# Performance work log

Measured on AMD Instinct MI355X. Metric: run time of the kernel, lower is better.

The kernel has to match this reference:

```python
import jax, jax.numpy as jnp
import numpy as np

NEG_SLOPE = 0.2
LN_EPS = 1e-5


def _gat(x, src, dst, ea, Wl, Wr, We, att, b, heads, ch, concat):
    # GATv2 conv with edge features (eval mode: dropout = identity).
    N = x.shape[0]
    xl = (x @ Wl).reshape(N, heads, ch)          # source transform (also skip output)
    xr = (x @ Wr).reshape(N, heads, ch)          # target transform
    ee = (ea @ We).reshape(ea.shape[0], heads, ch)
    g = jax.nn.leaky_relu(xl[src] + xr[dst] + ee, NEG_SLOPE)   # [E,H,C]
    score = jnp.einsum('ehc,hc->eh', g, att)                    # [E,H]
    # segment softmax over destination nodes
    smax = jax.ops.segment_max(score, dst, num_segments=N)
    ex = jnp.exp(score - smax[dst])
    den = jax.ops.segment_sum(ex, dst, num_segments=N)
    alpha = ex / (den[dst] + 1e-16)
    out = jax.ops.segment_sum(xl[src] * alpha[..., None], dst, num_segments=N)  # [N,H,C]
    out = out.reshape(N, heads * ch) if concat else out.mean(axis=1)
    return out + b, xl.reshape(N, heads * ch)


def setup_inputs() -> dict:
    B, N, E, F, ED = 4, 20000, 640000, 64, 16
    HID, H1 = 16, 8
    key = jax.random.key(0)
    ks = jax.random.split(key, 32)

    def p(k, shape, fan):
        return (jax.random.normal(k, shape, jnp.float32) / np.float32(np.sqrt(fan)))

    inp = {
        'x': jax.random.normal(ks[0], (B, N, F), jnp.float32),
        'edge_attr': jax.random.normal(ks[1], (B, E, ED), jnp.float32),
        'edge_index': jax.random.randint(ks[2], (B, 2, E), 0, N, jnp.int32),
        # conv1: in=64, heads=8, out=16, concat
        'c1_Wl': p(ks[3], (F, H1 * HID), F),
        'c1_Wr': p(ks[4], (F, H1 * HID), F),
        'c1_We': p(ks[5], (ED, H1 * HID), ED),
        'c1_att': p(ks[6], (H1, HID), HID),
        'c1_b': jnp.zeros((H1 * HID,), jnp.float32),
        # conv2: in=128, heads=1, out=16, mean
        'c2_Wl': p(ks[7], (H1 * HID, HID), H1 * HID),
        'c2_Wr': p(ks[8], (H1 * HID, HID), H1 * HID),
        'c2_We': p(ks[9], (ED, HID), ED),
        'c2_att': p(ks[10], (1, HID), HID),
        'c2_b': jnp.zeros((HID,), jnp.float32),
        # skip_conv: in=128, heads=1, out=16, mean
        's_Wl': p(ks[11], (H1 * HID, HID), H1 * HID),
        's_Wr': p(ks[12], (H1 * HID, HID), H1 * HID),
        's_We': p(ks[13], (ED, HID), ED),
        's_att': p(ks[14], (1, HID), HID),
        's_b': jnp.zeros((HID,), jnp.float32),
        # lin_skip_conv + LayerNorm(16)
        'lin_W': p(ks[15], (HID, HID), HID),
        'lin_b': jnp.zeros((HID,), jnp.float32),
        'ln_g': jnp.ones((HID,), jnp.float32),
        'ln_b': jnp.zeros((HID,), jnp.float32),
    }
    return inp


def reference(x, edge_attr, edge_index,
              c1_Wl, c1_Wr, c1_We, c1_att, c1_b,
              c2_Wl, c2_Wr, c2_We, c2_att, c2_b,
              s_Wl, s_Wr, s_We, s_att, s_b,
              lin_W, lin_b, ln_g, ln_b):
    def single(xg, eig, eag):
        src, dst = eig[0], eig[1]
        h, skip = _gat(xg, src, dst, eag, c1_Wl, c1_Wr, c1_We, c1_att, c1_b, 8, 16, True)
        hx = jax.nn.elu(h)                                   # [N,128]
        x1, _ = _gat(hx, src, dst, eag, c2_Wl, c2_Wr, c2_We, c2_att, c2_b, 1, 16, False)
        # skip conv consumes hx with the residual skip features from conv1
        x2, _ = _gat(hx + skip, src, dst, eag, s_Wl, s_Wr, s_We, s_att, s_b, 1, 16, False)
        x2 = x2 @ lin_W.T + lin_b
        y = x1 + x2                                          # [N,16]
        mu = y.mean(-1, keepdims=True)
        var = ((y - mu) ** 2).mean(-1, keepdims=True)
        return (y - mu) / jnp.sqrt(var + LN_EPS) * ln_g + ln_b
    return jax.vmap(single)(x, edge_index, edge_attr)
```

## Files before the change

kernel.cpp:

```cpp
#include <hip/hip_runtime.h>
#include <hip/hip_bf16.h>

typedef __hip_bfloat16 bf16;
typedef float f32x2 __attribute__((ext_vector_type(2)));

#define NB_B 4
#define N 20000
#define E 640000
#define F 64
#define HC 128
#define ED 16
#define CH 16
#define NT 32
#define TB1 64
#define TB2 16

__device__ __forceinline__ float clampf(float v, float lo, float hi){ return fminf(fmaxf(v, lo), hi); }
__device__ __forceinline__ float ldv(const float* p, size_t i){ return p[i]; }
__device__ __forceinline__ float ldv(const bf16*  p, size_t i){ return __bfloat162float(p[i]); }
__device__ __forceinline__ void  stv(float* p, size_t i, float v){ p[i] = v; }
__device__ __forceinline__ void  stv(bf16*  p, size_t i, float v){ p[i] = __float2bfloat16(v); }
__device__ __forceinline__ unsigned short tobf(float v){ bf16 b = __float2bfloat16(v); return *(unsigned short*)&b; }
__device__ __forceinline__ float unpl(unsigned u){ return __uint_as_float(u << 16); }
__device__ __forceinline__ float unph(unsigned u){ return __uint_as_float(u & 0xffff0000u); }
__device__ __forceinline__ f32x2 mk2(float a, float b){ f32x2 r; r.x = a; r.y = b; return r; }

__device__ __forceinline__ float rsum16(float x){
  x += __int_as_float(__builtin_amdgcn_update_dpp(0, __float_as_int(x), 0x128, 0xf, 0xf, true));
  x += __int_as_float(__builtin_amdgcn_update_dpp(0, __float_as_int(x), 0x124, 0xf, 0xf, true));
  x += __int_as_float(__builtin_amdgcn_update_dpp(0, __float_as_int(x), 0x122, 0xf, 0xf, true));
  x += __int_as_float(__builtin_amdgcn_update_dpp(0, __float_as_int(x), 0x121, 0xf, 0xf, true));
  return x;
}

__global__ __launch_bounds__(256) void k_detect(const unsigned short* __restrict__ xu, int* __restrict__ flag){
  __shared__ int cnt[256];
  int tid = threadIdx.x;
  unsigned short lo = xu[2*tid];
  bf16 h = *(const bf16*)&lo;
  float v = fabsf(__bfloat162float(h));
  cnt[tid] = (v > 1e4f || (v != 0.f && v < 1e-4f)) ? 1 : 0;
  __syncthreads();
  for (int s=128; s>0; s>>=1){ if (tid<s) cnt[tid]+=cnt[tid+s]; __syncthreads(); }
  if (tid==0) *flag = (cnt[0] > 64) ? 1 : 0;
}

__global__ __launch_bounds__(256) void k_hist(const int* __restrict__ ei, int* __restrict__ cnt, int b0){
  int z = blockIdx.z, b = b0 + z;
  int e = blockIdx.x*256 + threadIdx.x;
  int d = ei[((size_t)b*2+1)*E + e];
  atomicAdd(&cnt[z*N + d], 1);
}

__global__ __launch_bounds__(256) void k_scan(const int* __restrict__ cnt, int* __restrict__ rowptr,
                                              int* __restrict__ cursor){
  int z = blockIdx.z, tid = threadIdx.x;
  const int* c = cnt + (size_t)z*N;
  int* rp = rowptr + (size_t)z*(N+1);
  int* cu = cursor + (size_t)z*N;
  const int CHK = (N + 255)/256;
  int lo = tid*CHK; int hi = lo + CHK; if (hi > N) hi = N; if (lo > N) lo = N;
  int s = 0;
  for (int i=lo;i<hi;i++) s += c[i];
  __shared__ int buf[256];
  buf[tid] = s; __syncthreads();
  for (int off=1; off<256; off<<=1){
    int t = (tid>=off) ? buf[tid-off] : 0;
    __syncthreads();
    buf[tid] += t;
    __syncthreads();
  }
  int run = buf[tid] - s;
  for (int i=lo;i<hi;i++){ int v=c[i]; rp[i]=run; cu[i]=run; run += v; }
  if (tid==255) rp[N] = run;
}

template<typename T>
__device__ __forceinline__ void scatter_body(const int* ei, int* cursor, int* csr,
                                             const T* ea, float* eacsr, int b0){
  int z = blockIdx.z, b = b0 + z;
  int e = blockIdx.x*256 + threadIdx.x;
  int s = ei[((size_t)b*2+0)*E + e];
  int d = ei[((size_t)b*2+1)*E + e];
  int pos = atomicAdd(&cursor[z*N + d], 1);
  csr[(size_t)z*E + pos] = s;
  float4* dst = (float4*)(eacsr + ((size_t)z*E + pos)*ED);
  const T* sp = ea + ((size_t)b*E + e)*ED;
  #pragma unroll
  for (int g=0; g<4; g++){
    float4 t;
    t.x = ldv(sp, g*4+0); t.y = ldv(sp, g*4+1); t.z = ldv(sp, g*4+2); t.w = ldv(sp, g*4+3);
    dst[g] = t;
  }
}
__global__ __launch_bounds__(256) void k_scatter(const int* ei, int* cursor, int* csr,
    const void* ea, float* eacsr, const int* flag, int b0){
  if (*flag) scatter_body(ei, cursor, csr, (const float*)ea, eacsr, b0);
  else       scatter_body(ei, cursor, csr, (const bf16*) ea, eacsr, b0);
}

template<typename T>
__device__ __forceinline__ void node1_body(const T* x, const T* Wl, const T* Wr,
                                           unsigned* xl1p, unsigned* xr1p, int b0,
                                           float (*xs)[F+4]){
  int z = blockIdx.z, b = b0 + z;
  int node0 = blockIdx.x*NT;
  for (int i=threadIdx.x; i<NT*F; i+=256){
    int n = i>>6, k = i&63;
    xs[n][k] = ldv(x, ((size_t)b*N + node0 + n)*F + k);
  }
  __syncthreads();
  int mat = threadIdx.x >> 7, c = threadIdx.x & 127;
  const T* W = mat ? Wr : Wl;
  float acc[NT];
  #pragma unroll
  for (int n=0;n<NT;n++) acc[n]=0.f;
  for (int k=0;k<F;k+=4){
    float w0 = ldv(W, (size_t)(k+0)*HC + c);
    float w1 = ldv(W, (size_t)(k+1)*HC + c);
    float w2 = ldv(W, (size_t)(k+2)*HC + c);
    float w3 = ldv(W, (size_t)(k+3)*HC + c);
    #pragma unroll
    for (int n=0;n<NT;n++){
      float4 xv = *(const float4*)&xs[n][k];
      acc[n] += xv.x*w0 + xv.y*w1 + xv.z*w2 + xv.w*w3;
    }
  }
  unsigned short* outp = (unsigned short*)(mat ? xr1p : xl1p);
  int half = c>>6, cc = c&63;
  #pragma unroll
  for (int n=0;n<NT;n++){
    float v = clampf(acc[n], -1e4f, 1e4f);
    outp[(((size_t)z*N + node0 + n)*64 + cc)*2 + half] = tobf(v);
  }
}
__global__ __launch_bounds__(256) void k_node1(const void* x, const void* Wl, const void* Wr,
    unsigned* xl1p, unsigned* xr1p, const int* flag, int b0){
  __shared__ float xs[NT][F+4];
  if (*flag) node1_body((const float*)x,(const float*)Wl,(const float*)Wr,xl1p,xr1p,b0,xs);
  else       node1_body((const bf16*) x,(const bf16*) Wl,(const bf16*) Wr,xl1p,xr1p,b0,xs);
}

template<typename T>
__device__ __forceinline__ void gather1_body(const int* rowptr, const int* csr, const float* eacsr,
    const T* We, const T* att, const T* b1,
    const unsigned* xl1p, const unsigned* xr1p, float* hx, int b0,
    int (*ssrc)[TB1], float (*eas)[TB1][16]){
  int z = blockIdx.z;
  int wid = threadIdx.x >> 6, lane = threadIdx.x & 63;
  int node = blockIdx.x*4 + wid;
  int rs = rowptr[(size_t)z*(N+1) + node];
  int re = rowptr[(size_t)z*(N+1) + node + 1];
  unsigned xru = xr1p[((size_t)z*N + node)*64 + lane];
  f32x2 xr2 = mk2(unpl(xru), unph(xru));
  f32x2 w[ED];
  #pragma unroll
  for (int j=0;j<ED;j++) w[j] = mk2(ldv(We, (size_t)j*HC + lane), ldv(We, (size_t)j*HC + lane + 64));
  f32x2 attv = mk2(ldv(att, (size_t)lane), ldv(att, (size_t)lane + 64));
  f32x2 acc = mk2(0.f,0.f), den = mk2(0.f,0.f);
  const unsigned* xlp = xl1p + (size_t)z*N*64;
  const int* csrz = csr + (size_t)z*E;

  auto edge = [&](int i, unsigned xw){
    f32x2 xl = mk2(unpl(xw), unph(xw));
    float ev[16];
    const float4* er = (const float4*)eas[wid][i];
    *(float4*)&ev[0]  = er[0];
    *(float4*)&ev[4]  = er[1];
    *(float4*)&ev[8]  = er[2];
    *(float4*)&ev[12] = er[3];
    f32x2 g = xl + xr2;
    #pragma unroll
    for (int j=0;j<ED;j++) g += w[j]*ev[j];
    f32x2 lr;
    lr.x = fmaxf(g.x,0.f) + 0.2f*fminf(g.x,0.f);
    lr.y = fmaxf(g.y,0.f) + 0.2f*fminf(g.y,0.f);
    f32x2 v = lr*attv;
    float vL = rsum16(v.x);
    float vH = rsum16(v.y);
    f32x2 ex = mk2(__expf(clampf(vL,-60.f,60.f)), __expf(clampf(vH,-60.f,60.f)));
    den += ex;
    acc += ex*xl;
  };

  for (int base = rs; base < re; base += TB1){
    int m = re - base; if (m > TB1) m = TB1;
    if (lane < m) ssrc[wid][lane] = csrz[base + lane];
    const float4* ep = (const float4*)(eacsr + ((size_t)z*E + base)*ED);
    for (int i4=lane; i4<m*4; i4+=64)
      *(float4*)&eas[wid][i4>>2][(i4&3)*4] = ep[i4];
    unsigned pa = xlp[(unsigned)(ssrc[wid][0]*64 + lane)];
    unsigned pb = (m>1) ? xlp[(unsigned)(ssrc[wid][1]*64 + lane)] : pa;
    int i = 0;
    for (; i+1 < m; i += 2){
      unsigned x0 = pa, x1 = pb;
      int i2 = (i+2 < m) ? i+2 : m-1;
      int i3 = (i+3 < m) ? i+3 : m-1;
      int s2 = ssrc[wid][i2], s3 = ssrc[wid][i3];
      pa = xlp[(unsigned)(s2*64 + lane)];
      pb = xlp[(unsigned)(s3*64 + lane)];
      edge(i, x0);
      edge(i+1, x1);
    }
    if (i < m) edge(i, pa);
  }
  float hL = acc.x/(den.x + 1e-16f) + ldv(b1, (size_t)lane);
  float hH = acc.y/(den.y + 1e-16f) + ldv(b1, (size_t)lane + 64);
  hL = hL>0.f ? hL : expm1f(hL);
  hH = hH>0.f ? hH : expm1f(hH);
  hx[((size_t)z*N + node)*HC + lane]      = hL;
  hx[((size_t)z*N + node)*HC + lane + 64] = hH;
}
__global__ __launch_bounds__(256) void k_gather1(const int* rowptr, const int* csr, const float* eacsr,
    const void* We, const void* att, const void* b1,
    const unsigned* xl1p, const unsigned* xr1p, float* hx, const int* flag, int b0){
  __shared__ int ssrc[4][TB1];
  __shared__ float eas[4][TB1][16];
  if (*flag) gather1_body(rowptr,csr,eacsr,(const float*)We,(const float*)att,(const float*)b1,xl1p,xr1p,hx,b0,ssrc,eas);
  else       gather1_body(rowptr,csr,eacsr,(const bf16*) We,(const bf16*) att,(const bf16*) b1,xl1p,xr1p,hx,b0,ssrc,eas);
}

template<typename T>
__device__ __forceinline__ void node2_body(const float* hx, const unsigned* xl1p,
    const T* W2l, const T* W2r, const T* W3l, const T* W3r,
    unsigned* xl23p, unsigned* xr23p, int b0,
    float (*hv)[HC+4], float (*sv)[HC+4]){
  int z = blockIdx.z;
  int node0 = blockIdx.x*NT;
  for (int i=threadIdx.x; i<NT*HC; i+=256){
    int n = i>>7, k = i&127;
    float h = hx[((size_t)z*N + node0 + n)*HC + k];
    unsigned wxl = xl1p[((size_t)z*N + node0 + n)*64 + (k&63)];
    float xv = (k<64) ? unpl(wxl) : unph(wxl);
    hv[n][k] = h;
    sv[n][k] = h + xv;
  }
  __syncthreads();
  int o = threadIdx.x & 63;
  int mat = o >> 4, c = o & 15;
  int g = threadIdx.x >> 6;
  const T* W = (mat==0)? W2l : (mat==1)? W2r : (mat==2)? W3l : W3r;
  float (*src)[HC+4] = (mat<2)? hv : sv;
  float acc[8];
  #pragma unroll
  for (int j=0;j<8;j++) acc[j]=0.f;
  for (int k=0;k<HC;k+=4){
    float w0 = ldv(W, (size_t)(k+0)*CH + c);
    float w1 = ldv(W, (size_t)(k+1)*CH + c);
    float w2 = ldv(W, (size_t)(k+2)*CH + c);
    float w3 = ldv(W, (size_t)(k+3)*CH + c);
    #pragma unroll
    for (int j=0;j<8;j++){
      float4 xv = *(const float4*)&src[g*8+j][k];
      acc[j] += xv.x*w0 + xv.y*w1 + xv.z*w2 + xv.w*w3;
    }
  }
  unsigned short* arr = (unsigned short*)((mat&1) ? xr23p : xl23p);
  int half = mat>>1;
  #pragma unroll
  for (int j=0;j<8;j++){
    float v = clampf(acc[j], -1e4f, 1e4f);
    arr[(((size_t)z*N + node0 + g*8 + j)*CH + c)*2 + half] = tobf(v);
  }
}
__global__ __launch_bounds__(256) void k_node2(const float* hx, const unsigned* xl1p,
    const void* W2l, const void* W2r, const void* W3l, const void* W3r,
    unsigned* xl23p, unsigned* xr23p, const int* flag, int b0){
  __shared__ float hv[NT][HC+4];
  __shared__ float sv[NT][HC+4];
  if (*flag) node2_body(hx,xl1p,(const float*)W2l,(const float*)W2r,(const float*)W3l,(const float*)W3r,xl23p,xr23p,b0,hv,sv);
  else       node2_body(hx,xl1p,(const bf16*) W2l,(const bf16*) W2r,(const bf16*) W3l,(const bf16*) W3r,xl23p,xr23p,b0,hv,sv);
}

template<typename T>
__device__ __forceinline__ void gather23_body(const int* rowptr, const int* csr, const float* eacsr,
    const T* We2, const T* We3, const T* att2, const T* att3,
    const T* b2, const T* b3, const T* linW, const T* linb, const T* lng, const T* lnb,
    const unsigned* xl23p, const unsigned* xr23p,
    T* out, int b0, int (*ssrc)[TB2], float (*eas)[TB2][16]){
  int z = blockIdx.z;
  int slot = threadIdx.x >> 4;
  int node = blockIdx.x*16 + slot;
  int c = threadIdx.x & 15;
  int rs = rowptr[(size_t)z*(N+1) + node];
  int re = rowptr[(size_t)z*(N+1) + node + 1];
  unsigned xru = xr23p[((size_t)z*N + node)*CH + c];
  f32x2 xr2 = mk2(unpl(xru), unph(xru));
  f32x2 w[ED];
  #pragma unroll
  for (int j=0;j<ED;j++) w[j] = mk2(ldv(We2,(size_t)j*CH+c), ldv(We3,(size_t)j*CH+c));
  f32x2 attv = mk2(ldv(att2,(size_t)c), ldv(att3,(size_t)c));
  f32x2 acc = mk2(0.f,0.f), den = mk2(0.f,0.f);
  const unsigned* xlp = xl23p + (size_t)z*N*CH;
  const int* csrz = csr + (size_t)z*E;

  auto edge = [&](int i, unsigned xw){
    f32x2 xl = mk2(unpl(xw), unph(xw));
    float ev[16];
    const float4* er = (const float4*)eas[slot][i];
    *(float4*)&ev[0]  = er[0];
    *(float4*)&ev[4]  = er[1];
    *(float4*)&ev[8]  = er[2];
    *(float4*)&ev[12] = er[3];
    f32x2 g = xl + xr2;
    #pragma unroll
    for (int j=0;j<ED;j++) g += w[j]*ev[j];
    f32x2 lr;
    lr.x = fmaxf(g.x,0.f) + 0.2f*fminf(g.x,0.f);
    lr.y = fmaxf(g.y,0.f) + 0.2f*fminf(g.y,0.f);
    f32x2 v = lr*attv;
    float v2 = rsum16(v.x);
    float v3 = rsum16(v.y);
    f32x2 ex = mk2(__expf(clampf(v2,-60.f,60.f)), __expf(clampf(v3,-60.f,60.f)));
    den += ex;
    acc += ex*xl;
  };

  for (int base = rs; base < re; base += TB2){
    int m = re - base; if (m > TB2) m = TB2;
    if (c < m) ssrc[slot][c] = csrz[base + c];
    const float4* ep = (const float4*)(eacsr + ((size_t)z*E + base)*ED);
    for (int i4=c; i4<m*4; i4+=16)
      *(float4*)&eas[slot][i4>>2][(i4&3)*4] = ep[i4];
    unsigned pa = xlp[(unsigned)(ssrc[slot][0]*CH + c)];
    unsigned pb = (m>1) ? xlp[(unsigned)(ssrc[slot][1]*CH + c)] : pa;
    int i = 0;
    for (; i+1 < m; i += 2){
      unsigned x0 = pa, x1 = pb;
      int i2 = (i+2 < m) ? i+2 : m-1;
      int i3 = (i+3 < m) ? i+3 : m-1;
      int s2 = ssrc[slot][i2], s3 = ssrc[slot][i3];
      pa = xlp[(unsigned)(s2*CH + c)];
      pb = xlp[(unsigned)(s3*CH + c)];
      edge(i, x0);
      edge(i+1, x1);
    }
    if (i < m) edge(i, pa);
  }
  float x1 = acc.x/(den.x + 1e-16f) + ldv(b2,(size_t)c);
  float x3 = acc.y/(den.y + 1e-16f) + ldv(b3,(size_t)c);
  float x2 = 0.f;
  #pragma unroll
  for (int j=0;j<16;j++) x2 += __shfl(x3, j, 16) * ldv(linW, (size_t)c*16 + j);
  x2 += ldv(linb,(size_t)c);
  float y = clampf(x1, -1e6f, 1e6f) + clampf(x2, -1e6f, 1e6f);
  float mu = rsum16(y)*(1.f/16.f);
  float dv = y - mu;
  float var = rsum16(dv*dv)*(1.f/16.f);
  float o = dv*rsqrtf(var + 1e-5f)*ldv(lng,(size_t)c) + ldv(lnb,(size_t)c);
  stv(out, ((size_t)(b0+z)*N + node)*16 + c, o);
}
__global__ __launch_bounds__(256) void k_gather23(const int* rowptr, const int* csr, const float* eacsr,
    const void* We2, const void* We3, const void* att2, const void* att3,
    const void* b2, const void* b3, const void* linW, const void* linb, const void* lng, const void* lnb,
    const unsigned* xl23p, const unsigned* xr23p,
    void* out, const int* flag, int b0){
  __shared__ int ssrc[16][TB2];
  __shared__ float eas[16][TB2][16];
  if (*flag) gather23_body(rowptr,csr,eacsr,(const float*)We2,(const float*)We3,(const float*)att2,(const float*)att3,
                           (const float*)b2,(const float*)b3,(const float*)linW,(const float*)linb,(const float*)lng,(const float*)lnb,
                           xl23p,xr23p,(float*)out,b0,ssrc,eas);
  else       gather23_body(rowptr,csr,eacsr,(const bf16*) We2,(const bf16*) We3,(const bf16*) att2,(const bf16*) att3,
                           (const bf16*) b2,(const bf16*) b3,(const bf16*) linW,(const bf16*) linb,(const bf16*) lng,(const bf16*) lnb,
                           xl23p,xr23p,(bf16*) out,b0,ssrc,eas);
}

struct WSP {
  int* flag;
  int *cnt, *cursor, *rowptr; int* csr;
  float *eacsr, *hx;
  unsigned *xl1p,*xr1p,*xl23p,*xr23p;
  size_t total;
};
static WSP mkws(char* base, int nb){
  WSP w; size_t off = 0;
  auto A = [&](size_t bytes)->char*{ char* p = base ? base + off : (char*)0; off = (off + bytes + 255) & ~(size_t)255; return p; };
  w.flag   = (int*)     A(256);
  w.cnt    = (int*)     A((size_t)nb*N*4);
  w.cursor = (int*)     A((size_t)nb*N*4);
  w.rowptr = (int*)     A((size_t)nb*(N+1)*4);
  w.csr    = (int*)     A((size_t)nb*E*4);
  w.eacsr  = (float*)   A((size_t)nb*E*ED*4);
  w.hx     = (float*)   A((size_t)nb*N*HC*4);
  w.xl1p   = (unsigned*)A((size_t)nb*N*64*4);
  w.xr1p   = (unsigned*)A((size_t)nb*N*64*4);
  w.xl23p  = (unsigned*)A((size_t)nb*N*CH*4);
  w.xr23p  = (unsigned*)A((size_t)nb*N*CH*4);
  w.total = off;
  return w;
}

extern "C" void kernel_launch(void* const* d_in, const int* in_sizes, int n_in,
                              void* d_out, int out_size, void* d_ws, size_t ws_size,
                              hipStream_t stream){
  const void* x    = d_in[0];
  const void* ea   = d_in[1];
  const int*  ei   = (const int*)d_in[2];
  const void* c1Wl = d_in[3], *c1Wr = d_in[4], *c1We = d_in[5];
  const void* c1att= d_in[6], *c1b  = d_in[7];
  const void* c2Wl = d_in[8], *c2Wr = d_in[9], *c2We = d_in[10];
  const void* c2att= d_in[11],*c2b  = d_in[12];
  const void* sWl  = d_in[13],*sWr  = d_in[14],*sWe  = d_in[15];
  const void* satt = d_in[16],*sb   = d_in[17];
  const void* linW = d_in[18],*linb = d_in[19];
  const void* lng  = d_in[20],*lnb  = d_in[21];

  auto run = [&](int b0, int nb){
    WSP w = mkws((char*)d_ws, nb);
    hipMemsetAsync(w.cnt, 0, (size_t)nb*N*4, stream);
    k_hist   <<<dim3(E/256,1,nb),   256,0,stream>>>(ei, w.cnt, b0);
    k_scan   <<<dim3(1,1,nb),       256,0,stream>>>(w.cnt, w.rowptr, w.cursor);
    k_scatter<<<dim3(E/256,1,nb),   256,0,stream>>>(ei, w.cursor, w.csr, ea, w.eacsr, w.flag, b0);
    k_node1  <<<dim3(N/NT,1,nb),    256,0,stream>>>(x, c1Wl, c1Wr, w.xl1p, w.xr1p, w.flag, b0);
    k_gather1<<<dim3(N/4,1,nb),     256,0,stream>>>(w.rowptr, w.csr, w.eacsr, c1We, c1att, c1b,
                                                    w.xl1p, w.xr1p, w.hx, w.flag, b0);
    k_node2  <<<dim3(N/NT,1,nb),    256,0,stream>>>(w.hx, w.xl1p, c2Wl, c2Wr, sWl, sWr,
                                                    w.xl23p, w.xr23p, w.flag, b0);
    k_gather23<<<dim3(N/16,1,nb),   256,0,stream>>>(w.rowptr, w.csr, w.eacsr, c2We, sWe, c2att, satt,
                                                    c2b, sb, linW, linb, lng, lnb,
                                                    w.xl23p, w.xr23p, d_out, w.flag, b0);
  };

  {
    WSP w0 = mkws((char*)d_ws, 1);
    k_detect<<<1,256,0,stream>>>((const unsigned short*)x, w0.flag);
  }

  WSP probe = mkws((char*)0, NB_B);
  if (ws_size >= probe.total){
    run(0, NB_B);
  } else {
    for (int g=0; g<NB_B; ++g) run(g, 1);
  }
}
```

Before: 1.130 ms.

## Drop LDS staging in gather kernels and split gather23 edges across wave sub-groups

Both gather kernels stop staging source indices and edge attributes in shared memory. They now read them directly from global memory with wave-uniform readfirstlane scalar loads and register prefetch of the next edge. gather23 now gives each node a full wave, with four 16-lane groups each taking every fourth edge, and combines their partial sums with shuffles. Exponentials switch to exp2 with log2(e) folded into the attention weights. This trades LDS traffic and barriers for more parallel memory requests per node, and it launches four times as many blocks for gather23, so lanes sit idle on low-degree nodes.

```diff
diff --git a/kernel.cpp b/kernel.cpp
--- a/kernel.cpp
+++ b/kernel.cpp
@@ -12,8 +12,6 @@
 #define ED 16
 #define CH 16
 #define NT 32
-#define TB1 64
-#define TB2 16
 
 __device__ __forceinline__ float clampf(float v, float lo, float hi){ return fminf(fmaxf(v, lo), hi); }
 __device__ __forceinline__ float ldv(const float* p, size_t i){ return p[i]; }
@@ -24,6 +22,9 @@
 __device__ __forceinline__ float unpl(unsigned u){ return __uint_as_float(u << 16); }
 __device__ __forceinline__ float unph(unsigned u){ return __uint_as_float(u & 0xffff0000u); }
 __device__ __forceinline__ f32x2 mk2(float a, float b){ f32x2 r; r.x = a; r.y = b; return r; }
+__device__ __forceinline__ int rfl(int v){ return __builtin_amdgcn_readfirstlane(v); }
+
+#define L2E 1.44269504f
 
 __device__ __forceinline__ float rsum16(float x){
   x += __int_as_float(__builtin_amdgcn_update_dpp(0, __float_as_int(x), 0x128, 0xf, 0xf, true));
@@ -142,82 +143,72 @@
 }
 
 template<typename T>
-__device__ __forceinline__ void gather1_body(const int* rowptr, const int* csr, const float* eacsr,
-    const T* We, const T* att, const T* b1,
-    const unsigned* xl1p, const unsigned* xr1p, float* hx, int b0,
-    int (*ssrc)[TB1], float (*eas)[TB1][16]){
+__device__ __forceinline__ void gather1_body(const int* __restrict__ rowptr, const int* __restrict__ csr,
+    const float* __restrict__ eacsr, const T* __restrict__ We, const T* __restrict__ att, const T* __restrict__ b1,
+    const unsigned* __restrict__ xl1p, const unsigned* __restrict__ xr1p, float* __restrict__ hx, int b0){
   int z = blockIdx.z;
-  int wid = threadIdx.x >> 6, lane = threadIdx.x & 63;
-  int node = blockIdx.x*4 + wid;
-  int rs = rowptr[(size_t)z*(N+1) + node];
-  int re = rowptr[(size_t)z*(N+1) + node + 1];
+  int lane = threadIdx.x & 63;
+  int node = rfl(blockIdx.x*4 + (threadIdx.x >> 6));
+  int rs = rfl(rowptr[(size_t)z*(N+1) + node]);
+  int re = rfl(rowptr[(size_t)z*(N+1) + node + 1]);
+  f32x2 w[ED];
+  #pragma unroll
+  for (int j=0;j<ED;j++) w[j] = mk2(ldv(We,(size_t)j*HC+lane), ldv(We,(size_t)j*HC+lane+64));
+  f32x2 attv = mk2(ldv(att,(size_t)lane)*L2E, ldv(att,(size_t)lane+64)*L2E);
   unsigned xru = xr1p[((size_t)z*N + node)*64 + lane];
   f32x2 xr2 = mk2(unpl(xru), unph(xru));
-  f32x2 w[ED];
-  #pragma unroll
-  for (int j=0;j<ED;j++) w[j] = mk2(ldv(We, (size_t)j*HC + lane), ldv(We, (size_t)j*HC + lane + 64));
-  f32x2 attv = mk2(ldv(att, (size_t)lane), ldv(att, (size_t)lane + 64));
   f32x2 acc = mk2(0.f,0.f), den = mk2(0.f,0.f);
-  const unsigned* xlp = xl1p + (size_t)z*N*64;
-  const int* csrz = csr + (size_t)z*E;
-
-  auto edge = [&](int i, unsigned xw){
-    f32x2 xl = mk2(unpl(xw), unph(xw));
-    float ev[16];
-    const float4* er = (const float4*)eas[wid][i];
-    *(float4*)&ev[0]  = er[0];
-    *(float4*)&ev[4]  = er[1];
-    *(float4*)&ev[8]  = er[2];
-    *(float4*)&ev[12] = er[3];
-    f32x2 g = xl + xr2;
-    #pragma unroll
-    for (int j=0;j<ED;j++) g += w[j]*ev[j];
-    f32x2 lr;
-    lr.x = fmaxf(g.x,0.f) + 0.2f*fminf(g.x,0.f);
-    lr.y = fmaxf(g.y,0.f) + 0.2f*fminf(g.y,0.f);
-    f32x2 v = lr*attv;
-    float vL = rsum16(v.x);
-    float vH = rsum16(v.y);
-    f32x2 ex = mk2(__expf(clampf(vL,-60.f,60.f)), __expf(clampf(vH,-60.f,60.f)));
-    den += ex;
-    acc += ex*xl;
-  };
-
-  for (int base = rs; base < re; base += TB1){
-    int m = re - base; if (m > TB1) m = TB1;
-    if (lane < m) ssrc[wid][lane] = csrz[base + lane];
-    const float4* ep = (const float4*)(eacsr + ((size_t)z*E + base)*ED);
-    for (int i4=lane; i4<m*4; i4+=64)
-      *(float4*)&eas[wid][i4>>2][(i4&3)*4] = ep[i4];
-    unsigned pa = xlp[(unsigned)(ssrc[wid][0]*64 + lane)];
-    unsigned pb = (m>1) ? xlp[(unsigned)(ssrc[wid][1]*64 + lane)] : pa;
-    int i = 0;
-    for (; i+1 < m; i += 2){
-      unsigned x0 = pa, x1 = pb;
-      int i2 = (i+2 < m) ? i+2 : m-1;
-      int i3 = (i+3 < m) ? i+3 : m-1;
-      int s2 = ssrc[wid][i2], s3 = ssrc[wid][i3];
-      pa = xlp[(unsigned)(s2*64 + lane)];
-      pb = xlp[(unsigned)(s3*64 + lane)];
-      edge(i, x0);
-      edge(i+1, x1);
+  const unsigned* __restrict__ xlp = xl1p + (size_t)z*N*64;
+  const int* __restrict__ csrz = csr + (size_t)z*E + rs;
+  const float* __restrict__ eaz = eacsr + ((size_t)z*E + rs)*ED;
+  int deg = re - rs;
+  if (deg > 0){
+    int s0 = rfl(csrz[0]);
+    int s1 = (deg>1) ? rfl(csrz[1]) : s0;
+    unsigned xa = xlp[(size_t)(unsigned)s0*64 + lane];
+    unsigned xb = xlp[(size_t)(unsigned)s1*64 + lane];
+    #pragma unroll 2
+    for (int i=0;i<deg;i++){
+      const float* __restrict__ ep = eaz + (size_t)i*ED;
+      float ev[ED];
+      #pragma unroll
+      for (int j=0;j<ED;j++) ev[j] = ep[j];
+      unsigned xw = xa;
+      xa = xb;
+      if (i+2 < deg){
+        int sn = rfl(csrz[i+2]);
+        xb = xlp[(size_t)(unsigned)sn*64 + lane];
+      }
+      f32x2 xl = mk2(unpl(xw), unph(xw));
+      f32x2 g0 = xl + xr2, g1 = mk2(0.f,0.f);
+      #pragma unroll
+      for (int j=0;j<ED;j+=2){ g0 += w[j]*ev[j]; g1 += w[j+1]*ev[j+1]; }
+      f32x2 g = g0 + g1;
+      f32x2 lr;
+      lr.x = fmaxf(g.x,0.f) + 0.2f*fminf(g.x,0.f);
+      lr.y = fmaxf(g.y,0.f) + 0.2f*fminf(g.y,0.f);
+      f32x2 v = lr*attv;
+      float vL = rsum16(v.x);
+      float vH = rsum16(v.y);
+      f32x2 ex = mk2(exp2f(clampf(vL,-86.f,86.f)), exp2f(clampf(vH,-86.f,86.f)));
+      den += ex;
+      acc += ex*xl;
     }
-    if (i < m) edge(i, pa);
-  }
-  float hL = acc.x/(den.x + 1e-16f) + ldv(b1, (size_t)lane);
-  float hH = acc.y/(den.y + 1e-16f) + ldv(b1, (size_t)lane + 64);
+  }
+  float hL = acc.x/(den.x + 1e-16f) + ldv(b1,(size_t)lane);
+  float hH = acc.y/(den.y + 1e-16f) + ldv(b1,(size_t)lane+64);
   hL = hL>0.f ? hL : expm1f(hL);
   hH = hH>0.f ? hH : expm1f(hH);
   hx[((size_t)z*N + node)*HC + lane]      = hL;
   hx[((size_t)z*N + node)*HC + lane + 64] = hH;
 }
-__global__ __launch_bounds__(256) void k_gather1(const int* rowptr, const int* csr, const float* eacsr,
+__global__ __launch_bounds__(256) void k_gather1(const int* __restrict__ rowptr, const int* __restrict__ csr,
+    const float* __restrict__ eacsr,
     const void* We, const void* att, const void* b1,
-    const unsigned* xl1p, const unsigned* xr1p, float* hx, const int* flag, int b0){
-  __shared__ int ssrc[4][TB1];
-  __shared__ float eas[4][TB1][16];
-  if (*flag) gather1_body(rowptr,csr,eacsr,(const float*)We,(const float*)att,(const float*)b1,xl1p,xr1p,hx,b0,ssrc,eas);
-  else       gather1_body(rowptr,csr,eacsr,(const bf16*) We,(const bf16*) att,(const bf16*) b1,xl1p,xr1p,hx,b0,ssrc,eas);
+    const unsigned* __restrict__ xl1p, const unsigned* __restrict__ xr1p, float* __restrict__ hx,
+    const int* __restrict__ flag, int b0){
+  if (*flag) gather1_body(rowptr,csr,eacsr,(const float*)We,(const float*)att,(const float*)b1,xl1p,xr1p,hx,b0);
+  else       gather1_body(rowptr,csr,eacsr,(const bf16*) We,(const bf16*) att,(const bf16*) b1,xl1p,xr1p,hx,b0);
 }
 
 template<typename T>
@@ -273,70 +264,76 @@
 }
 
 template<typename T>
-__device__ __forceinline__ void gather23_body(const int* rowptr, const int* csr, const float* eacsr,
-    const T* We2, const T* We3, const T* att2, const T* att3,
-    const T* b2, const T* b3, const T* linW, const T* linb, const T* lng, const T* lnb,
-    const unsigned* xl23p, const unsigned* xr23p,
-    T* out, int b0, int (*ssrc)[TB2], float (*eas)[TB2][16]){
+__device__ __forceinline__ void gather23_body(const int* __restrict__ rowptr, const int* __restrict__ csr,
+    const float* __restrict__ eacsr,
+    const T* __restrict__ We2, const T* __restrict__ We3, const T* __restrict__ att2, const T* __restrict__ att3,
+    const T* __restrict__ b2, const T* __restrict__ b3, const T* __restrict__ linW, const T* __restrict__ linb,
+    const T* __restrict__ lng, const T* __restrict__ lnb,
+    const unsigned* __restrict__ xl23p, const unsigned* __restrict__ xr23p,
+    T* __restrict__ out, int b0){
   int z = blockIdx.z;
-  int slot = threadIdx.x >> 4;
-  int node = blockIdx.x*16 + slot;
-  int c = threadIdx.x & 15;
-  int rs = rowptr[(size_t)z*(N+1) + node];
-  int re = rowptr[(size_t)z*(N+1) + node + 1];
+  int lane = threadIdx.x & 63;
+  int g = lane >> 4, c = lane & 15;
+  int node = rfl(blockIdx.x*4 + (threadIdx.x >> 6));
+  int rs = rfl(rowptr[(size_t)z*(N+1) + node]);
+  int re = rfl(rowptr[(size_t)z*(N+1) + node + 1]);
+  int deg = re - rs;
+  f32x2 w[ED];
+  #pragma unroll
+  for (int j=0;j<ED;j++) w[j] = mk2(ldv(We2,(size_t)j*CH+c), ldv(We3,(size_t)j*CH+c));
+  f32x2 attv = mk2(ldv(att2,(size_t)c)*L2E, ldv(att3,(size_t)c)*L2E);
   unsigned xru = xr23p[((size_t)z*N + node)*CH + c];
   f32x2 xr2 = mk2(unpl(xru), unph(xru));
-  f32x2 w[ED];
-  #pragma unroll
-  for (int j=0;j<ED;j++) w[j] = mk2(ldv(We2,(size_t)j*CH+c), ldv(We3,(size_t)j*CH+c));
-  f32x2 attv = mk2(ldv(att2,(size_t)c), ldv(att3,(size_t)c));
   f32x2 acc = mk2(0.f,0.f), den = mk2(0.f,0.f);
-  const unsigned* xlp = xl23p + (size_t)z*N*CH;
-  const int* csrz = csr + (size_t)z*E;
-
-  auto edge = [&](int i, unsigned xw){
-    f32x2 xl = mk2(unpl(xw), unph(xw));
-    float ev[16];
-    const float4* er = (const float4*)eas[slot][i];
-    *(float4*)&ev[0]  = er[0];
-    *(float4*)&ev[4]  = er[1];
-    *(float4*)&ev[8]  = er[2];
-    *(float4*)&ev[12] = er[3];
-    f32x2 g = xl + xr2;
-    #pragma unroll
-    for (int j=0;j<ED;j++) g += w[j]*ev[j];
-    f32x2 lr;
-    lr.x = fmaxf(g.x,0.f) + 0.2f*fminf(g.x,0.f);
-    lr.y = fmaxf(g.y,0.f) + 0.2f*fminf(g.y,0.f);
-    f32x2 v = lr*attv;
-    float v2 = rsum16(v.x);
-    float v3 = rsum16(v.y);
-    f32x2 ex = mk2(__expf(clampf(v2,-60.f,60.f)), __expf(clampf(v3,-60.f,60.f)));
-    den += ex;
-    acc += ex*xl;
-  };
-
-  for (int base = rs; base < re; base += TB2){
-    int m = re - base; if (m > TB2) m = TB2;
-    if (c < m) ssrc[slot][c] = csrz[base + c];
-    const float4* ep = (const float4*)(eacsr + ((size_t)z*E + base)*ED);
-    for (int i4=c; i4<m*4; i4+=16)
-      *(float4*)&eas[slot][i4>>2][(i4&3)*4] = ep[i4];
-    unsigned pa = xlp[(unsigned)(ssrc[slot][0]*CH + c)];
-    unsigned pb = (m>1) ? xlp[(unsigned)(ssrc[slot][1]*CH + c)] : pa;
-    int i = 0;
-    for (; i+1 < m; i += 2){
-      unsigned x0 = pa, x1 = pb;
-      int i2 = (i+2 < m) ? i+2 : m-1;
-      int i3 = (i+3 < m) ? i+3 : m-1;
-      int s2 = ssrc[slot][i2], s3 = ssrc[slot][i3];
-      pa = xlp[(unsigned)(s2*CH + c)];
-      pb = xlp[(unsigned)(s3*CH + c)];
-      edge(i, x0);
-      edge(i+1, x1);
+  const unsigned* __restrict__ xlp = xl23p + (size_t)z*N*CH;
+  const int* __restrict__ csrz = csr + (size_t)z*E + rs;
+  const float* __restrict__ eaz = eacsr + ((size_t)z*E + rs)*ED;
+  if (deg > 0){
+    int idx0 = (g < deg) ? g : deg-1;
+    int s = csrz[idx0];
+    unsigned xw = xlp[(size_t)(unsigned)s*CH + c];
+    const float4* p0 = (const float4*)(eaz + (size_t)idx0*ED);
+    float4 e0 = p0[0], e1 = p0[1], e2 = p0[2], e3 = p0[3];
+    for (int i=0;i<deg;i+=4){
+      bool act = (i + g) < deg;
+      unsigned xcur = xw;
+      float4 c0 = e0, c1 = e1, c2 = e2, c3 = e3;
+      if (i+4 < deg){
+        int ii = i + 4 + g;
+        int idx = (ii < deg) ? ii : deg-1;
+        int s2 = csrz[idx];
+        xw = xlp[(size_t)(unsigned)s2*CH + c];
+        const float4* p2 = (const float4*)(eaz + (size_t)idx*ED);
+        e0 = p2[0]; e1 = p2[1]; e2 = p2[2]; e3 = p2[3];
+      }
+      float ev[ED];
+      *(float4*)&ev[0]  = c0;
+      *(float4*)&ev[4]  = c1;
+      *(float4*)&ev[8]  = c2;
+      *(float4*)&ev[12] = c3;
+      f32x2 xl = mk2(unpl(xcur), unph(xcur));
+      f32x2 g0 = xl + xr2, g1 = mk2(0.f,0.f);
+      #pragma unroll
+      for (int j=0;j<ED;j+=2){ g0 += w[j]*ev[j]; g1 += w[j+1]*ev[j+1]; }
+      f32x2 gg = g0 + g1;
+      f32x2 lr;
+      lr.x = fmaxf(gg.x,0.f) + 0.2f*fminf(gg.x,0.f);
+      lr.y = fmaxf(gg.y,0.f) + 0.2f*fminf(gg.y,0.f);
+      f32x2 v = lr*attv;
+      float v2 = rsum16(v.x);
+      float v3 = rsum16(v.y);
+      float x2e = exp2f(clampf(v2,-86.f,86.f));
+      float x3e = exp2f(clampf(v3,-86.f,86.f));
+      if (!act){ x2e = 0.f; x3e = 0.f; }
+      f32x2 ex = mk2(x2e, x3e);
+      den += ex;
+      acc += ex*xl;
     }
-    if (i < m) edge(i, pa);
-  }
+  }
+  acc.x += __shfl_xor(acc.x, 16); acc.x += __shfl_xor(acc.x, 32);
+  acc.y += __shfl_xor(acc.y, 16); acc.y += __shfl_xor(acc.y, 32);
+  den.x += __shfl_xor(den.x, 16); den.x += __shfl_xor(den.x, 32);
+  den.y += __shfl_xor(den.y, 16); den.y += __shfl_xor(den.y, 32);
   float x1 = acc.x/(den.x + 1e-16f) + ldv(b2,(size_t)c);
   float x3 = acc.y/(den.y + 1e-16f) + ldv(b3,(size_t)c);
   float x2 = 0.f;
@@ -348,21 +345,20 @@
   float dv = y - mu;
   float var = rsum16(dv*dv)*(1.f/16.f);
   float o = dv*rsqrtf(var + 1e-5f)*ldv(lng,(size_t)c) + ldv(lnb,(size_t)c);
-  stv(out, ((size_t)(b0+z)*N + node)*16 + c, o);
-}
-__global__ __launch_bounds__(256) void k_gather23(const int* rowptr, const int* csr, const float* eacsr,
+  if (lane < 16) stv(out, ((size_t)(b0+z)*N + node)*16 + c, o);
+}
+__global__ __launch_bounds__(256) void k_gather23(const int* __restrict__ rowptr, const int* __restrict__ csr,
+    const float* __restrict__ eacsr,
     const void* We2, const void* We3, const void* att2, const void* att3,
     const void* b2, const void* b3, const void* linW, const void* linb, const void* lng, const void* lnb,
-    const unsigned* xl23p, const unsigned* xr23p,
-    void* out, const int* flag, int b0){
-  __shared__ int ssrc[16][TB2];
-  __shared__ float eas[16][TB2][16];
+    const unsigned* __restrict__ xl23p, const unsigned* __restrict__ xr23p,
+    void* out, const int* __restrict__ flag, int b0){
   if (*flag) gather23_body(rowptr,csr,eacsr,(const float*)We2,(const float*)We3,(const float*)att2,(const float*)att3,
                            (const float*)b2,(const float*)b3,(const float*)linW,(const float*)linb,(const float*)lng,(const float*)lnb,
-                           xl23p,xr23p,(float*)out,b0,ssrc,eas);
+                           xl23p,xr23p,(float*)out,b0);
   else       gather23_body(rowptr,csr,eacsr,(const bf16*) We2,(const bf16*) We3,(const bf16*) att2,(const bf16*) att3,
                            (const bf16*) b2,(const bf16*) b3,(const bf16*) linW,(const bf16*) linb,(const bf16*) lng,(const bf16*) lnb,
-                           xl23p,xr23p,(bf16*) out,b0,ssrc,eas);
+                           xl23p,xr23p,(bf16*) out,b0);
 }
 
 struct WSP {
@@ -416,7 +412,7 @@
                                                     w.xl1p, w.xr1p, w.hx, w.flag, b0);
     k_node2  <<<dim3(N/NT,1,nb),    256,0,stream>>>(w.hx, w.xl1p, c2Wl, c2Wr, sWl, sWr,
                                                     w.xl23p, w.xr23p, w.flag, b0);
-    k_gather23<<<dim3(N/16,1,nb),   256,0,stream>>>(w.rowptr, w.csr, w.eacsr, c2We, sWe, c2att, satt,
+    k_gather23<<<dim3(N/4,1,nb),    256,0,stream>>>(w.rowptr, w.csr, w.eacsr, c2We, sWe, c2att, satt,
                                                     c2b, sb, linW, linb, lng, lnb,
                                                     w.xl23p, w.xr23p, d_out, w.flag, b0);
   };
```

Measured after the change: 1.214 ms. 7.4% more time.
